# Kernel optimization log

Measured on AMD Instinct MI355X. Metric: run time of the kernel, lower is better.

## Reference

```python
import jax, jax.numpy as jnp
import numpy as np

C = 256
NUM_HEADS = 8
HEAD_DIM = C // NUM_HEADS


def setup_inputs() -> dict:
    key = jax.random.key(0)
    ks = jax.random.split(key, 12)
    d = {}
    d["x"] = jax.random.normal(ks[0], (1, C, 16, 32, 32), dtype=jnp.float32)
    # temporal conv: Conv3d kernel (3,1,1) -> store as [C_out, C_in, 3]
    d["tc_w"] = jax.random.normal(ks[1], (C, C, 3), dtype=jnp.float32) * 0.02
    d["tc_b"] = jnp.zeros((C,), dtype=jnp.float32)
    # 1x1x1 conv3d projections == per-channel linear, store as [C_out, C_in]
    for i, n in enumerate(["q", "k", "v", "o"]):
        d[n + "_w"] = jax.random.normal(ks[2 + i], (C, C), dtype=jnp.float32) * 0.02
        d[n + "_b"] = jnp.zeros((C,), dtype=jnp.float32)
    # learned temporal positional embedding [1, C, 16, 1, 1]
    d["pos_emb"] = jax.random.normal(ks[10], (1, C, 16, 1, 1), dtype=jnp.float32) * 0.02
    return d


def _proj(w, b, y):
    # 1x1x1 Conv3d == channel-mixing linear on [B,C,T,H,W]
    return jnp.einsum('oc,bcthw->bothw', w, y) + b[None, :, None, None, None]


def _forward(x, tc_w, tc_b, q_w, q_b, k_w, k_b, v_w, v_b, o_w, o_b, pos_emb):
    B, Cc, T, H, W = x.shape
    nh, hd = NUM_HEADS, Cc // NUM_HEADS
    # ---- temporal_conv: Conv3d kernel (3,1,1), padding (1,0,0) ----
    x4 = x.reshape(B, Cc, T, H * W)
    local = jax.lax.conv_general_dilated(
        x4, tc_w[:, :, :, None], window_strides=(1, 1),
        padding=((1, 1), (0, 0)),
        dimension_numbers=('NCHW', 'OIHW', 'NCHW'))
    local = local.reshape(B, Cc, T, H, W) + tc_b[None, :, None, None, None]
    # ---- temporal attention (per-frame spatial attention) ----
    xp = x + pos_emb[:, :, :T]  # T <= 16, plain slice
    q = _proj(q_w, q_b, xp)
    k = _proj(k_w, k_b, xp)
    v = _proj(v_w, v_b, xp)

    def heads(y):  # [B,C,T,H,W] -> [B,nh,T,P,hd]
        return y.reshape(B, nh, hd, T, H * W).transpose(0, 1, 3, 4, 2)

    q, k, v = heads(q), heads(k), heads(v)
    scale = hd ** -0.5
    attn = jax.nn.softmax(jnp.einsum('bntpd,bntqd->bntpq', q, k) * scale, axis=-1)
    out = jnp.einsum('bntpq,bntqd->bntpd', attn, v)
    out = out.transpose(0, 1, 4, 2, 3).reshape(B, Cc, T, H, W)  # b (n d) t h w
    out = _proj(o_w, o_b, out)
    return local + out


def reference(x, tc_w, tc_b, q_w, q_b, k_w, k_b, v_w, v_b, o_w, o_b, pos_emb):
    return _forward(x, tc_w, tc_b, q_w, q_b, k_w, k_b, v_w, v_b, o_w, o_b, pos_emb)
```

## Files before the change

### kernel.cpp

```cpp
#include <hip/hip_runtime.h>
#include <hip/hip_bf16.h>


typedef __bf16 bf16x8 __attribute__((ext_vector_type(8)));
typedef float  f32x4  __attribute__((ext_vector_type(4)));

__device__ __forceinline__ ushort f2bf(float f) {
    union { float f; unsigned int u; } x; x.f = f;
    unsigned int r = x.u + 0x7FFFu + ((x.u >> 16) & 1u);
    return (ushort)(r >> 16);
}

__device__ __forceinline__ bf16x8 ldg8(const ushort* p) {
    union { int4 i; bf16x8 b; } u;
    u.i = *reinterpret_cast<const int4*>(p);
    return u.b;
}

#define SCL_QK 0.25504600765996234f

__global__ __launch_bounds__(256)
void prep_all(const float* __restrict__ x, const float* __restrict__ pos,
              const float* __restrict__ qw, const float* __restrict__ kw,
              const float* __restrict__ vw, const float* __restrict__ ow,
              const float* __restrict__ tcw,
              const float* __restrict__ qb, const float* __restrict__ kb,
              const float* __restrict__ vb, const float* __restrict__ ob,
              const float* __restrict__ tcb,
              ushort* __restrict__ xpt, ushort* __restrict__ wqkv,
              ushort* __restrict__ wfin, float* __restrict__ bqkv,
              float* __restrict__ bfin)
{
    const int b   = blockIdx.x;
    const int tid = threadIdx.x;
    if (b < 1024) {
        __shared__ float tile[64][65];
        const int tp0 = (b & 255) * 64;
        const int c0  = (b >> 8) * 64;
        {
            const int j = tid & 63, i0 = (tid >> 6) * 16;
            #pragma unroll
            for (int rr = 0; rr < 16; ++rr) {
                int i = i0 + rr;
                tile[i][j] = x[(size_t)(c0 + i) * 16384 + tp0 + j];
            }
        }
        __syncthreads();
        {
            const int ii = tid & 63, jj0 = (tid >> 6) * 16;
            #pragma unroll
            for (int rr = 0; rr < 16; ++rr) {
                int jj = jj0 + rr;
                int c = c0 + ii, tp = tp0 + jj;
                int t = tp >> 10;
                xpt[(size_t)tp * 256 + c] = f2bf(tile[ii][jj] + pos[c * 16 + t]);
            }
        }
    } else if (b < 1280) {
        __shared__ float red[256][16];
        const int o = b - 1024;
        const int c = tid;
        const float w0 = tcw[o * 768 + c * 3 + 0];
        const float w1 = tcw[o * 768 + c * 3 + 1];
        const float w2 = tcw[o * 768 + c * 3 + 2];
        float p[16];
        #pragma unroll
        for (int t = 0; t < 16; ++t) p[t] = pos[c * 16 + t];
        #pragma unroll
        for (int t = 0; t < 16; ++t) {
            float pm1 = (t > 0)  ? p[t - 1] : 0.f;
            float pp1 = (t < 15) ? p[t + 1] : 0.f;
            red[c][t] = w0 * pm1 + w1 * p[t] + w2 * pp1;
        }
        __syncthreads();
        #pragma unroll
        for (int s = 128; s >= 1; s >>= 1) {
            if (c < s)
                #pragma unroll
                for (int t = 0; t < 16; ++t) red[c][t] += red[c + s][t];
            __syncthreads();
        }
        if (c < 16) bfin[c * 256 + o] = ob[o] + tcb[o] - red[0][c];
    } else {
        int i = (b - 1280) * 256 + tid;
        if (i < 196608) {
            int m = i >> 8, k = i & 255;
            float val = (m < 256) ? qw[m * 256 + k]
                      : (m < 512) ? kw[(m - 256) * 256 + k]
                                  : vw[(m - 512) * 256 + k];
            wqkv[i] = f2bf(val);
        } else if (i < 458752) {
            int p = i - 196608;
            int o = p >> 10, col = p & 1023;
            float val;
            if (col < 256) val = ow[o * 256 + col];
            else { int q = col - 256; int c = q & 255, kseg = q >> 8;
                   val = tcw[o * 768 + c * 3 + kseg]; }
            wfin[p] = f2bf(val);
        } else if (i < 459520) {
            int bq = i - 458752;
            bqkv[bq] = (bq < 256) ? qb[bq] : (bq < 512) ? kb[bq - 256] : vb[bq - 512];
        }
    }
}

template<int MODE>
__global__ __launch_bounds__(256)
void gemm_bt(const ushort* __restrict__ A, const ushort* __restrict__ B,
             const ushort* __restrict__ B2,
             void* __restrict__ outp, void* __restrict__ outp2,
             const float* __restrict__ bias,
             const int M, const int N, const int K)
{
    __shared__ __align__(16) ushort As[128][72];
    __shared__ __align__(16) ushort Bs[64][72];

    const int tid  = threadIdx.x;
    const int lane = tid & 63;
    const int w    = tid >> 6;
    const int lr   = lane & 15;
    const int hk   = lane >> 4;

    const int n0 = blockIdx.x * 64;
    const int m0 = blockIdx.y * 128;
    const int wm = w * 32;

    const int srow = tid >> 3;
    const int scol = (tid & 7) * 8;

    f32x4 acc[2][4] = {};

    for (int kk0 = 0; kk0 < K; kk0 += 64) {
        const int seg  = kk0 >> 8;
        const int bcol = kk0 & 255;
        const ushort* bs = B;
        bool ok = true;
        if constexpr (MODE == 3) {
            if (seg != 0) {
                int tf = (n0 >> 10) + seg - 2;
                ok = ((unsigned)tf < 16u);
                bs = B2 + (((ptrdiff_t)seg - 2) << 18);
            }
        }
        __syncthreads();
        #pragma unroll
        for (int q = 0; q < 4; ++q) {
            const int row = srow + q * 32;
            *reinterpret_cast<int4*>(&As[row][scol]) =
                *reinterpret_cast<const int4*>(A + (size_t)(m0 + row) * K + kk0 + scol);
        }
        if (ok) {
            #pragma unroll
            for (int q = 0; q < 2; ++q) {
                const int row = srow + q * 32;
                *reinterpret_cast<int4*>(&Bs[row][scol]) =
                    *reinterpret_cast<const int4*>(bs + (size_t)(n0 + row) * 256 + bcol + scol);
            }
        } else {
            #pragma unroll
            for (int q = 0; q < 2; ++q)
                *reinterpret_cast<int4*>(&Bs[srow + q * 32][scol]) = make_int4(0, 0, 0, 0);
        }
        __syncthreads();
        #pragma unroll
        for (int ks = 0; ks < 2; ++ks) {
            bf16x8 af[2], bfr[4];
            #pragma unroll
            for (int mi = 0; mi < 2; ++mi)
                af[mi] = *reinterpret_cast<const bf16x8*>(&As[wm + mi * 16 + lr][ks * 32 + hk * 8]);
            #pragma unroll
            for (int nj = 0; nj < 4; ++nj)
                bfr[nj] = *reinterpret_cast<const bf16x8*>(&Bs[nj * 16 + lr][ks * 32 + hk * 8]);
            #pragma unroll
            for (int mi = 0; mi < 2; ++mi)
                #pragma unroll
                for (int nj = 0; nj < 4; ++nj)
                    acc[mi][nj] = __builtin_amdgcn_mfma_f32_16x16x32_bf16(af[mi], bfr[nj], acc[mi][nj], 0, 0, 0);
        }
    }

    const float* bb = bias;
    if constexpr (MODE == 3) bb = bias + ((n0 >> 10) << 8);

    #pragma unroll
    for (int mi = 0; mi < 2; ++mi) {
        const int mb = m0 + wm + mi * 16 + hk * 4;
        const float b0 = bb[mb + 0], b1 = bb[mb + 1], b2 = bb[mb + 2], b3 = bb[mb + 3];
        #pragma unroll
        for (int nj = 0; nj < 4; ++nj) {
            const int n = n0 + nj * 16 + lr;
            const f32x4 a = acc[mi][nj];
            if constexpr (MODE == 0) {
                if (mb < 512) {
                    const float sc = (mb < 256) ? SCL_QK : 1.0f;
                    ushort4 pk;
                    pk.x = f2bf((a[0] + b0) * sc); pk.y = f2bf((a[1] + b1) * sc);
                    pk.z = f2bf((a[2] + b2) * sc); pk.w = f2bf((a[3] + b3) * sc);
                    ushort* o = (ushort*)outp;
                    size_t base = (size_t)(mb >> 8) * (8ull * 16384 * 32)
                                + (size_t)((mb >> 5) & 7) * (16384ull * 32)
                                + (mb & 31);
                    *reinterpret_cast<ushort4*>(o + base + (size_t)n * 32) = pk;
                } else {
                    int c = mb - 512;
                    ushort* o = (ushort*)outp2;
                    o[(size_t)(c + 0) * 16384 + n] = f2bf(a[0] + b0);
                    o[(size_t)(c + 1) * 16384 + n] = f2bf(a[1] + b1);
                    o[(size_t)(c + 2) * 16384 + n] = f2bf(a[2] + b2);
                    o[(size_t)(c + 3) * 16384 + n] = f2bf(a[3] + b3);
                }
            } else {
                float* o = (float*)outp;
                o[(size_t)(mb + 0) * N + n] = a[0] + b0;
                o[(size_t)(mb + 1) * N + n] = a[1] + b1;
                o[(size_t)(mb + 2) * N + n] = a[2] + b2;
                o[(size_t)(mb + 3) * N + n] = a[3] + b3;
            }
        }
    }
}

__global__ __launch_bounds__(256, 4)
void attn_kernel(const ushort* __restrict__ qhd, const ushort* __restrict__ v,
                 ushort* __restrict__ outp)
{
    const int lane = threadIdx.x & 63;
    const int w    = threadIdx.x >> 6;
    const int lr   = lane & 15;
    const int hk   = lane >> 4;

    const int prob = blockIdx.x;
    const int qb   = blockIdx.y;
    const int hn   = prob >> 4, t = prob & 15;

    const ushort* qh = qhd + (size_t)hn * (16384 * 32);
    const ushort* kh = qhd + 8ull * 16384 * 32 + (size_t)hn * (16384 * 32);

    const int p0 = qb * 128 + w * 32;
    const size_t rowbase = (size_t)t * 1024;

    const ushort* kbase = kh + (rowbase + lr) * 32 + hk * 8;
    const ushort* vbase = v + (size_t)(hn * 32 + lr) * 16384 + rowbase + hk * 8;

    bf16x8 qf[2];
    #pragma unroll
    for (int mi = 0; mi < 2; ++mi)
        qf[mi] = ldg8(qh + (rowbase + p0 + mi * 16 + lr) * 32 + hk * 8);

    union { ushort s[8]; bf16x8 v; } onesu;
    #pragma unroll
    for (int j = 0; j < 8; ++j) onesu.s[j] = 0x3F80;
    const bf16x8 ones = onesu.v;

    f32x4 o_acc[2][2] = {};
    f32x4 lsum[2] = {};

    for (int kv0 = 0; kv0 < 1024; kv0 += 64) {
        bf16x8 vf[2][2];
        #pragma unroll
        for (int kq = 0; kq < 2; ++kq)
            #pragma unroll
            for (int nf = 0; nf < 2; ++nf)
                vf[kq][nf] = ldg8(vbase + (size_t)nf * 262144 + kv0 + kq * 32);
        bf16x8 kf[4];
        #pragma unroll
        for (int nj = 0; nj < 4; ++nj)
            kf[nj] = ldg8(kbase + (size_t)(kv0 + nj * 16) * 32);
        f32x4 s[4][2] = {};
        #pragma unroll
        for (int nj = 0; nj < 4; ++nj)
            #pragma unroll
            for (int mi = 0; mi < 2; ++mi)
                s[nj][mi] = __builtin_amdgcn_mfma_f32_16x16x32_bf16(kf[nj], qf[mi], s[nj][mi], 0, 0, 0);
        uint u[2][8];
        #pragma unroll
        for (int mi = 0; mi < 2; ++mi) {
            float ps[16];
            #pragma unroll
            for (int nj = 0; nj < 4; ++nj)
                #pragma unroll
                for (int r = 0; r < 4; ++r)
                    ps[nj * 4 + r] = exp2f(s[nj][mi][r]);
            #pragma unroll
            for (int j = 0; j < 8; ++j)
                asm("v_cvt_pk_bf16_f32 %0, %1, %2" : "=v"(u[mi][j]) : "v"(ps[2 * j]), "v"(ps[2 * j + 1]));
            asm("v_permlane32_swap_b32 %0, %1" : "+v"(u[mi][0]), "+v"(u[mi][2]));
            asm("v_permlane32_swap_b32 %0, %1" : "+v"(u[mi][1]), "+v"(u[mi][3]));
            asm("v_permlane16_swap_b32 %0, %1" : "+v"(u[mi][0]), "+v"(u[mi][2]));
            asm("v_permlane16_swap_b32 %0, %1" : "+v"(u[mi][1]), "+v"(u[mi][3]));
            asm("v_permlane32_swap_b32 %0, %1" : "+v"(u[mi][4]), "+v"(u[mi][6]));
            asm("v_permlane32_swap_b32 %0, %1" : "+v"(u[mi][5]), "+v"(u[mi][7]));
            asm("v_permlane16_swap_b32 %0, %1" : "+v"(u[mi][4]), "+v"(u[mi][6]));
            asm("v_permlane16_swap_b32 %0, %1" : "+v"(u[mi][5]), "+v"(u[mi][7]));
        }
        #pragma unroll
        for (int kq = 0; kq < 2; ++kq) {
            #pragma unroll
            for (int mi = 0; mi < 2; ++mi) {
                union { uint4 i; bf16x8 b; } pu;
                pu.i = make_uint4(u[mi][kq * 4 + 0], u[mi][kq * 4 + 1],
                                  u[mi][kq * 4 + 2], u[mi][kq * 4 + 3]);
                lsum[mi] = __builtin_amdgcn_mfma_f32_16x16x32_bf16(pu.b, ones, lsum[mi], 0, 0, 0);
                #pragma unroll
                for (int nf = 0; nf < 2; ++nf)
                    o_acc[mi][nf] = __builtin_amdgcn_mfma_f32_16x16x32_bf16(pu.b, vf[kq][nf], o_acc[mi][nf], 0, 0, 0);
            }
        }
    }

    #pragma unroll
    for (int mi = 0; mi < 2; ++mi) {
        float inv[4];
        #pragma unroll
        for (int r = 0; r < 4; ++r) inv[r] = 1.f / lsum[mi][r];
        #pragma unroll
        for (int nf = 0; nf < 2; ++nf)
            #pragma unroll
            for (int r = 0; r < 4; ++r)
                outp[(rowbase + p0 + mi * 16 + hk * 4 + r) * 256 + hn * 32 + nf * 16 + lr] =
                    f2bf(o_acc[mi][nf][r] * inv[r]);
    }
}

extern "C" void kernel_launch(void* const* d_in, const int* in_sizes, int n_in,
                              void* d_out, int out_size, void* d_ws, size_t ws_size,
                              hipStream_t stream)
{
    const float* x   = (const float*)d_in[0];
    const float* tcw = (const float*)d_in[1];
    const float* tcb = (const float*)d_in[2];
    const float* qw  = (const float*)d_in[3];
    const float* qb  = (const float*)d_in[4];
    const float* kw  = (const float*)d_in[5];
    const float* kb  = (const float*)d_in[6];
    const float* vw  = (const float*)d_in[7];
    const float* vb  = (const float*)d_in[8];
    const float* ow  = (const float*)d_in[9];
    const float* ob  = (const float*)d_in[10];
    const float* pos = (const float*)d_in[11];

    char* ws = (char*)d_ws;
    size_t off = 0;
    auto alloc = [&](size_t bytes) {
        void* p = ws + off;
        off += (bytes + 255) & ~(size_t)255;
        return p;
    };
    ushort* xpt   = (ushort*)alloc(16384ull * 256 * 2);
    ushort* qkhd  = (ushort*)alloc(2ull * 8 * 16384 * 32 * 2);
    ushort* vbuf  = (ushort*)alloc(256ull * 16384 * 2);
    ushort* attnb = (ushort*)alloc(16384ull * 256 * 2);
    ushort* wqkv  = (ushort*)alloc(768ull * 256 * 2);
    ushort* wfin  = (ushort*)alloc(256ull * 1024 * 2);
    float*  bqkv  = (float*)alloc(768 * 4);
    float*  bfin  = (float*)alloc(16ull * 256 * 4);

    prep_all<<<3075, 256, 0, stream>>>(x, pos, qw, kw, vw, ow, tcw, qb, kb, vb, ob, tcb,
                                       xpt, wqkv, wfin, bqkv, bfin);

    gemm_bt<0><<<dim3(256, 6), 256, 0, stream>>>(wqkv, xpt, nullptr, qkhd, vbuf, bqkv,
                                                 768, 16384, 256);

    attn_kernel<<<dim3(128, 8), 256, 0, stream>>>(qkhd, vbuf, attnb);

    gemm_bt<3><<<dim3(256, 2), 256, 0, stream>>>(wfin, attnb, xpt, (float*)d_out, nullptr, bfin,
                                                 256, 16384, 1024);
}
```

Measured before the change: 102.4 us.

## Halve per-wave query rows in attention and vectorize prep transpose

Each attention wave now handles 16 query rows instead of 32 and the grid doubles to 128x16 blocks. This cuts register pressure and raises parallelism, but every K/V tile is now read from global memory twice as often per query. Separately, the x transpose in prep_all uses float4 loads and ushort4 packed stores, and the positional embedding is loaded once per thread instead of once per element.

```diff
diff --git a/kernel.cpp b/kernel.cpp
--- a/kernel.cpp
+++ b/kernel.cpp
@@ -37,23 +37,36 @@
         __shared__ float tile[64][65];
         const int tp0 = (b & 255) * 64;
         const int c0  = (b >> 8) * 64;
+        const int t   = tp0 >> 10;
         {
-            const int j = tid & 63, i0 = (tid >> 6) * 16;
-            #pragma unroll
-            for (int rr = 0; rr < 16; ++rr) {
-                int i = i0 + rr;
-                tile[i][j] = x[(size_t)(c0 + i) * 16384 + tp0 + j];
+            const int j4 = (tid & 15) * 4;
+            const int i0 = tid >> 4;
+            #pragma unroll
+            for (int rr = 0; rr < 4; ++rr) {
+                int i = rr * 16 + i0;
+                float4 vv = *reinterpret_cast<const float4*>(
+                    &x[(size_t)(c0 + i) * 16384 + tp0 + j4]);
+                tile[i][j4 + 0] = vv.x; tile[i][j4 + 1] = vv.y;
+                tile[i][j4 + 2] = vv.z; tile[i][j4 + 3] = vv.w;
             }
         }
         __syncthreads();
         {
-            const int ii = tid & 63, jj0 = (tid >> 6) * 16;
-            #pragma unroll
-            for (int rr = 0; rr < 16; ++rr) {
-                int jj = jj0 + rr;
-                int c = c0 + ii, tp = tp0 + jj;
-                int t = tp >> 10;
-                xpt[(size_t)tp * 256 + c] = f2bf(tile[ii][jj] + pos[c * 16 + t]);
+            const int cq = (tid & 15) * 4;
+            const int i0 = tid >> 4;
+            float pv0 = pos[(c0 + cq + 0) * 16 + t];
+            float pv1 = pos[(c0 + cq + 1) * 16 + t];
+            float pv2 = pos[(c0 + cq + 2) * 16 + t];
+            float pv3 = pos[(c0 + cq + 3) * 16 + t];
+            #pragma unroll
+            for (int rr = 0; rr < 4; ++rr) {
+                int jj = rr * 16 + i0;
+                ushort4 pk;
+                pk.x = f2bf(tile[cq + 0][jj] + pv0);
+                pk.y = f2bf(tile[cq + 1][jj] + pv1);
+                pk.z = f2bf(tile[cq + 2][jj] + pv2);
+                pk.w = f2bf(tile[cq + 3][jj] + pv3);
+                *reinterpret_cast<ushort4*>(&xpt[(size_t)(tp0 + jj) * 256 + c0 + cq]) = pk;
             }
         }
     } else if (b < 1280) {
@@ -236,90 +249,77 @@
     const ushort* qh = qhd + (size_t)hn * (16384 * 32);
     const ushort* kh = qhd + 8ull * 16384 * 32 + (size_t)hn * (16384 * 32);
 
-    const int p0 = qb * 128 + w * 32;
+    const int p0 = qb * 64 + w * 16;
     const size_t rowbase = (size_t)t * 1024;
 
-    const ushort* kbase = kh + (rowbase + lr) * 32 + hk * 8;
-    const ushort* vbase = v + (size_t)(hn * 32 + lr) * 16384 + rowbase + hk * 8;
-
-    bf16x8 qf[2];
-    #pragma unroll
-    for (int mi = 0; mi < 2; ++mi)
-        qf[mi] = ldg8(qh + (rowbase + p0 + mi * 16 + lr) * 32 + hk * 8);
+    const ushort* kptr  = kh + (rowbase + lr) * 32 + hk * 8;
+    const ushort* vptr0 = v + (size_t)(hn * 32 + lr) * 16384 + rowbase + hk * 8;
+    const ushort* vptr1 = vptr0 + 262144;
+
+    bf16x8 qf = ldg8(qh + (rowbase + p0 + lr) * 32 + hk * 8);
 
     union { ushort s[8]; bf16x8 v; } onesu;
     #pragma unroll
     for (int j = 0; j < 8; ++j) onesu.s[j] = 0x3F80;
     const bf16x8 ones = onesu.v;
 
-    f32x4 o_acc[2][2] = {};
-    f32x4 lsum[2] = {};
-
-    for (int kv0 = 0; kv0 < 1024; kv0 += 64) {
+    f32x4 o_acc[2] = {};
+    f32x4 lsum = {};
+    const f32x4 fzero = {};
+
+    for (int it = 0; it < 16; ++it) {
         bf16x8 vf[2][2];
         #pragma unroll
-        for (int kq = 0; kq < 2; ++kq)
-            #pragma unroll
-            for (int nf = 0; nf < 2; ++nf)
-                vf[kq][nf] = ldg8(vbase + (size_t)nf * 262144 + kv0 + kq * 32);
+        for (int kq = 0; kq < 2; ++kq) {
+            vf[kq][0] = ldg8(vptr0 + kq * 32);
+            vf[kq][1] = ldg8(vptr1 + kq * 32);
+        }
         bf16x8 kf[4];
         #pragma unroll
         for (int nj = 0; nj < 4; ++nj)
-            kf[nj] = ldg8(kbase + (size_t)(kv0 + nj * 16) * 32);
-        f32x4 s[4][2] = {};
+            kf[nj] = ldg8(kptr + nj * 512);
+        f32x4 s[4];
         #pragma unroll
         for (int nj = 0; nj < 4; ++nj)
-            #pragma unroll
-            for (int mi = 0; mi < 2; ++mi)
-                s[nj][mi] = __builtin_amdgcn_mfma_f32_16x16x32_bf16(kf[nj], qf[mi], s[nj][mi], 0, 0, 0);
-        uint u[2][8];
-        #pragma unroll
-        for (int mi = 0; mi < 2; ++mi) {
-            float ps[16];
-            #pragma unroll
-            for (int nj = 0; nj < 4; ++nj)
-                #pragma unroll
-                for (int r = 0; r < 4; ++r)
-                    ps[nj * 4 + r] = exp2f(s[nj][mi][r]);
-            #pragma unroll
-            for (int j = 0; j < 8; ++j)
-                asm("v_cvt_pk_bf16_f32 %0, %1, %2" : "=v"(u[mi][j]) : "v"(ps[2 * j]), "v"(ps[2 * j + 1]));
-            asm("v_permlane32_swap_b32 %0, %1" : "+v"(u[mi][0]), "+v"(u[mi][2]));
-            asm("v_permlane32_swap_b32 %0, %1" : "+v"(u[mi][1]), "+v"(u[mi][3]));
-            asm("v_permlane16_swap_b32 %0, %1" : "+v"(u[mi][0]), "+v"(u[mi][2]));
-            asm("v_permlane16_swap_b32 %0, %1" : "+v"(u[mi][1]), "+v"(u[mi][3]));
-            asm("v_permlane32_swap_b32 %0, %1" : "+v"(u[mi][4]), "+v"(u[mi][6]));
-            asm("v_permlane32_swap_b32 %0, %1" : "+v"(u[mi][5]), "+v"(u[mi][7]));
-            asm("v_permlane16_swap_b32 %0, %1" : "+v"(u[mi][4]), "+v"(u[mi][6]));
-            asm("v_permlane16_swap_b32 %0, %1" : "+v"(u[mi][5]), "+v"(u[mi][7]));
-        }
+            s[nj] = __builtin_amdgcn_mfma_f32_16x16x32_bf16(kf[nj], qf, fzero, 0, 0, 0);
+        float ps[16];
+        #pragma unroll
+        for (int nj = 0; nj < 4; ++nj)
+            #pragma unroll
+            for (int r = 0; r < 4; ++r)
+                ps[nj * 4 + r] = exp2f(s[nj][r]);
+        uint u[8];
+        #pragma unroll
+        for (int j = 0; j < 8; ++j)
+            asm("v_cvt_pk_bf16_f32 %0, %1, %2" : "=v"(u[j]) : "v"(ps[2 * j]), "v"(ps[2 * j + 1]));
+        asm("v_permlane32_swap_b32 %0, %1" : "+v"(u[0]), "+v"(u[2]));
+        asm("v_permlane32_swap_b32 %0, %1" : "+v"(u[1]), "+v"(u[3]));
+        asm("v_permlane16_swap_b32 %0, %1" : "+v"(u[0]), "+v"(u[2]));
+        asm("v_permlane16_swap_b32 %0, %1" : "+v"(u[1]), "+v"(u[3]));
+        asm("v_permlane32_swap_b32 %0, %1" : "+v"(u[4]), "+v"(u[6]));
+        asm("v_permlane32_swap_b32 %0, %1" : "+v"(u[5]), "+v"(u[7]));
+        asm("v_permlane16_swap_b32 %0, %1" : "+v"(u[4]), "+v"(u[6]));
+        asm("v_permlane16_swap_b32 %0, %1" : "+v"(u[5]), "+v"(u[7]));
         #pragma unroll
         for (int kq = 0; kq < 2; ++kq) {
-            #pragma unroll
-            for (int mi = 0; mi < 2; ++mi) {
-                union { uint4 i; bf16x8 b; } pu;
-                pu.i = make_uint4(u[mi][kq * 4 + 0], u[mi][kq * 4 + 1],
-                                  u[mi][kq * 4 + 2], u[mi][kq * 4 + 3]);
-                lsum[mi] = __builtin_amdgcn_mfma_f32_16x16x32_bf16(pu.b, ones, lsum[mi], 0, 0, 0);
-                #pragma unroll
-                for (int nf = 0; nf < 2; ++nf)
-                    o_acc[mi][nf] = __builtin_amdgcn_mfma_f32_16x16x32_bf16(pu.b, vf[kq][nf], o_acc[mi][nf], 0, 0, 0);
-            }
-        }
+            union { uint4 i; bf16x8 b; } pu;
+            pu.i = make_uint4(u[kq * 4 + 0], u[kq * 4 + 1], u[kq * 4 + 2], u[kq * 4 + 3]);
+            lsum = __builtin_amdgcn_mfma_f32_16x16x32_bf16(pu.b, ones, lsum, 0, 0, 0);
+            o_acc[0] = __builtin_amdgcn_mfma_f32_16x16x32_bf16(pu.b, vf[kq][0], o_acc[0], 0, 0, 0);
+            o_acc[1] = __builtin_amdgcn_mfma_f32_16x16x32_bf16(pu.b, vf[kq][1], o_acc[1], 0, 0, 0);
+        }
+        kptr += 2048; vptr0 += 64; vptr1 += 64;
     }
 
+    float inv[4];
     #pragma unroll
-    for (int mi = 0; mi < 2; ++mi) {
-        float inv[4];
-        #pragma unroll
-        for (int r = 0; r < 4; ++r) inv[r] = 1.f / lsum[mi][r];
-        #pragma unroll
-        for (int nf = 0; nf < 2; ++nf)
-            #pragma unroll
-            for (int r = 0; r < 4; ++r)
-                outp[(rowbase + p0 + mi * 16 + hk * 4 + r) * 256 + hn * 32 + nf * 16 + lr] =
-                    f2bf(o_acc[mi][nf][r] * inv[r]);
-    }
+    for (int r = 0; r < 4; ++r) inv[r] = 1.f / lsum[r];
+    #pragma unroll
+    for (int nf = 0; nf < 2; ++nf)
+        #pragma unroll
+        for (int r = 0; r < 4; ++r)
+            outp[(rowbase + p0 + hk * 4 + r) * 256 + hn * 32 + nf * 16 + lr] =
+                f2bf(o_acc[nf][r] * inv[r]);
 }
 
 extern "C" void kernel_launch(void* const* d_in, const int* in_sizes, int n_in,
@@ -361,7 +361,7 @@
     gemm_bt<0><<<dim3(256, 6), 256, 0, stream>>>(wqkv, xpt, nullptr, qkhd, vbuf, bqkv,
                                                  768, 16384, 256);
 
-    attn_kernel<<<dim3(128, 8), 256, 0, stream>>>(qkhd, vbuf, attnb);
+    attn_kernel<<<dim3(128, 16), 256, 0, stream>>>(qkhd, vbuf, attnb);
 
     gemm_bt<3><<<dim3(256, 2), 256, 0, stream>>>(wfin, attnb, xpt, (float*)d_out, nullptr, bfin,
                                                  256, 16384, 1024);
```

Result: slower. 143.5 us (+40.1%).

## Split attention KV range across two wave groups and vectorize prep transpose

Applied to the files above, without the earlier changes.

The attention kernel now launches 512 threads per block: two groups of four waves each process half of the 1024 keys, and the partial output accumulators and row sums are combined through shared memory before normalization. The goal is more waves in flight and a shorter serial KV loop per wave, which should hide more load latency, at the cost of an LDS reduction, a barrier, and half the waves idling during the epilogue. Separately, the input transpose in prep_all uses float4 loads and ushort4 packed stores, and hoists the positional-embedding loads out of the loop, to cut memory transactions.

```diff
diff --git a/kernel.cpp b/kernel.cpp
--- a/kernel.cpp
+++ b/kernel.cpp
@@ -37,23 +37,36 @@
         __shared__ float tile[64][65];
         const int tp0 = (b & 255) * 64;
         const int c0  = (b >> 8) * 64;
+        const int t   = tp0 >> 10;
         {
-            const int j = tid & 63, i0 = (tid >> 6) * 16;
-            #pragma unroll
-            for (int rr = 0; rr < 16; ++rr) {
-                int i = i0 + rr;
-                tile[i][j] = x[(size_t)(c0 + i) * 16384 + tp0 + j];
+            const int j4 = (tid & 15) * 4;
+            const int i0 = tid >> 4;
+            #pragma unroll
+            for (int rr = 0; rr < 4; ++rr) {
+                int i = rr * 16 + i0;
+                float4 vv = *reinterpret_cast<const float4*>(
+                    &x[(size_t)(c0 + i) * 16384 + tp0 + j4]);
+                tile[i][j4 + 0] = vv.x; tile[i][j4 + 1] = vv.y;
+                tile[i][j4 + 2] = vv.z; tile[i][j4 + 3] = vv.w;
             }
         }
         __syncthreads();
         {
-            const int ii = tid & 63, jj0 = (tid >> 6) * 16;
-            #pragma unroll
-            for (int rr = 0; rr < 16; ++rr) {
-                int jj = jj0 + rr;
-                int c = c0 + ii, tp = tp0 + jj;
-                int t = tp >> 10;
-                xpt[(size_t)tp * 256 + c] = f2bf(tile[ii][jj] + pos[c * 16 + t]);
+            const int cq = (tid & 15) * 4;
+            const int i0 = tid >> 4;
+            float pv0 = pos[(c0 + cq + 0) * 16 + t];
+            float pv1 = pos[(c0 + cq + 1) * 16 + t];
+            float pv2 = pos[(c0 + cq + 2) * 16 + t];
+            float pv3 = pos[(c0 + cq + 3) * 16 + t];
+            #pragma unroll
+            for (int rr = 0; rr < 4; ++rr) {
+                int jj = rr * 16 + i0;
+                ushort4 pk;
+                pk.x = f2bf(tile[cq + 0][jj] + pv0);
+                pk.y = f2bf(tile[cq + 1][jj] + pv1);
+                pk.z = f2bf(tile[cq + 2][jj] + pv2);
+                pk.w = f2bf(tile[cq + 3][jj] + pv3);
+                *reinterpret_cast<ushort4*>(&xpt[(size_t)(tp0 + jj) * 256 + c0 + cq]) = pk;
             }
         }
     } else if (b < 1280) {
@@ -220,12 +233,17 @@
     }
 }
 
-__global__ __launch_bounds__(256, 4)
+__global__ __launch_bounds__(512, 4)
 void attn_kernel(const ushort* __restrict__ qhd, const ushort* __restrict__ v,
                  ushort* __restrict__ outp)
 {
-    const int lane = threadIdx.x & 63;
-    const int w    = threadIdx.x >> 6;
+    __shared__ float comb[4][24][64];
+
+    const int tid  = threadIdx.x;
+    const int lane = tid & 63;
+    const int w    = tid >> 6;
+    const int ws   = w & 3;
+    const int kvh  = w >> 2;
     const int lr   = lane & 15;
     const int hk   = lane >> 4;
 
@@ -236,11 +254,13 @@
     const ushort* qh = qhd + (size_t)hn * (16384 * 32);
     const ushort* kh = qhd + 8ull * 16384 * 32 + (size_t)hn * (16384 * 32);
 
-    const int p0 = qb * 128 + w * 32;
+    const int p0 = qb * 128 + ws * 32;
     const size_t rowbase = (size_t)t * 1024;
-
-    const ushort* kbase = kh + (rowbase + lr) * 32 + hk * 8;
-    const ushort* vbase = v + (size_t)(hn * 32 + lr) * 16384 + rowbase + hk * 8;
+    const int kv0 = kvh * 512;
+
+    const ushort* kptr  = kh + (rowbase + kv0 + lr) * 32 + hk * 8;
+    const ushort* vptr0 = v + (size_t)(hn * 32 + lr) * 16384 + rowbase + kv0 + hk * 8;
+    const ushort* vptr1 = vptr0 + 262144;
 
     bf16x8 qf[2];
     #pragma unroll
@@ -254,24 +274,22 @@
 
     f32x4 o_acc[2][2] = {};
     f32x4 lsum[2] = {};
-
-    for (int kv0 = 0; kv0 < 1024; kv0 += 64) {
+    const f32x4 fzero = {};
+
+    for (int it = 0; it < 8; ++it) {
         bf16x8 vf[2][2];
-        #pragma unroll
-        for (int kq = 0; kq < 2; ++kq)
-            #pragma unroll
-            for (int nf = 0; nf < 2; ++nf)
-                vf[kq][nf] = ldg8(vbase + (size_t)nf * 262144 + kv0 + kq * 32);
+        vf[0][0] = ldg8(vptr0);      vf[0][1] = ldg8(vptr1);
+        vf[1][0] = ldg8(vptr0 + 32); vf[1][1] = ldg8(vptr1 + 32);
         bf16x8 kf[4];
         #pragma unroll
         for (int nj = 0; nj < 4; ++nj)
-            kf[nj] = ldg8(kbase + (size_t)(kv0 + nj * 16) * 32);
-        f32x4 s[4][2] = {};
+            kf[nj] = ldg8(kptr + nj * 512);
+        f32x4 s[4][2];
         #pragma unroll
         for (int nj = 0; nj < 4; ++nj)
             #pragma unroll
             for (int mi = 0; mi < 2; ++mi)
-                s[nj][mi] = __builtin_amdgcn_mfma_f32_16x16x32_bf16(kf[nj], qf[mi], s[nj][mi], 0, 0, 0);
+                s[nj][mi] = __builtin_amdgcn_mfma_f32_16x16x32_bf16(kf[nj], qf[mi], fzero, 0, 0, 0);
         uint u[2][8];
         #pragma unroll
         for (int mi = 0; mi < 2; ++mi) {
@@ -301,24 +319,51 @@
                 pu.i = make_uint4(u[mi][kq * 4 + 0], u[mi][kq * 4 + 1],
                                   u[mi][kq * 4 + 2], u[mi][kq * 4 + 3]);
                 lsum[mi] = __builtin_amdgcn_mfma_f32_16x16x32_bf16(pu.b, ones, lsum[mi], 0, 0, 0);
-                #pragma unroll
-                for (int nf = 0; nf < 2; ++nf)
-                    o_acc[mi][nf] = __builtin_amdgcn_mfma_f32_16x16x32_bf16(pu.b, vf[kq][nf], o_acc[mi][nf], 0, 0, 0);
-            }
-        }
-    }
-
-    #pragma unroll
-    for (int mi = 0; mi < 2; ++mi) {
-        float inv[4];
-        #pragma unroll
-        for (int r = 0; r < 4; ++r) inv[r] = 1.f / lsum[mi][r];
-        #pragma unroll
-        for (int nf = 0; nf < 2; ++nf)
+                o_acc[mi][0] = __builtin_amdgcn_mfma_f32_16x16x32_bf16(pu.b, vf[kq][0], o_acc[mi][0], 0, 0, 0);
+                o_acc[mi][1] = __builtin_amdgcn_mfma_f32_16x16x32_bf16(pu.b, vf[kq][1], o_acc[mi][1], 0, 0, 0);
+            }
+        }
+        kptr += 2048; vptr0 += 64; vptr1 += 64;
+    }
+
+    if (kvh == 1) {
+        #pragma unroll
+        for (int mi = 0; mi < 2; ++mi) {
+            #pragma unroll
+            for (int nf = 0; nf < 2; ++nf)
+                #pragma unroll
+                for (int r = 0; r < 4; ++r)
+                    comb[ws][mi * 8 + nf * 4 + r][lane] = o_acc[mi][nf][r];
             #pragma unroll
             for (int r = 0; r < 4; ++r)
-                outp[(rowbase + p0 + mi * 16 + hk * 4 + r) * 256 + hn * 32 + nf * 16 + lr] =
-                    f2bf(o_acc[mi][nf][r] * inv[r]);
+                comb[ws][16 + mi * 4 + r][lane] = lsum[mi][r];
+        }
+    }
+    __syncthreads();
+    if (kvh == 0) {
+        #pragma unroll
+        for (int mi = 0; mi < 2; ++mi) {
+            #pragma unroll
+            for (int nf = 0; nf < 2; ++nf)
+                #pragma unroll
+                for (int r = 0; r < 4; ++r)
+                    o_acc[mi][nf][r] += comb[ws][mi * 8 + nf * 4 + r][lane];
+            #pragma unroll
+            for (int r = 0; r < 4; ++r)
+                lsum[mi][r] += comb[ws][16 + mi * 4 + r][lane];
+        }
+        #pragma unroll
+        for (int mi = 0; mi < 2; ++mi) {
+            float inv[4];
+            #pragma unroll
+            for (int r = 0; r < 4; ++r) inv[r] = 1.f / lsum[mi][r];
+            #pragma unroll
+            for (int nf = 0; nf < 2; ++nf)
+                #pragma unroll
+                for (int r = 0; r < 4; ++r)
+                    outp[(rowbase + p0 + mi * 16 + hk * 4 + r) * 256 + hn * 32 + nf * 16 + lr] =
+                        f2bf(o_acc[mi][nf][r] * inv[r]);
+        }
     }
 }
 
@@ -361,7 +406,7 @@
     gemm_bt<0><<<dim3(256, 6), 256, 0, stream>>>(wqkv, xpt, nullptr, qkhd, vbuf, bqkv,
                                                  768, 16384, 256);
 
-    attn_kernel<<<dim3(128, 8), 256, 0, stream>>>(qkhd, vbuf, attnb);
+    attn_kernel<<<dim3(128, 8), 512, 0, stream>>>(qkhd, vbuf, attnb);
 
     gemm_bt<3><<<dim3(256, 2), 256, 0, stream>>>(wfin, attnb, xpt, (float*)d_out, nullptr, bfin,
                                                  256, 16384, 1024);
```

Measured after the change: 104.4 us. Within noise of the previous version (+2.0%).
